# Optimization experiments

Measured on AMD Instinct MI355X. Metric: run time of the kernel, lower is better.

The kernel has to match this reference:

```python
import jax, jax.numpy as jnp
import numpy as np

N_EMB = 1024
HEAD = 64
BLOCK = 2048
BATCH = 8


def setup_inputs() -> dict:
    key = jax.random.key(0)
    k_in, k_q, k_k, k_v = jax.random.split(key, 4)
    inp = jax.random.normal(k_in, (BATCH, BLOCK, N_EMB), dtype=jnp.float32)
    s = 1.0 / np.sqrt(N_EMB)
    Wq = jax.random.uniform(k_q, (N_EMB, HEAD), dtype=jnp.float32, minval=-s, maxval=s)
    Wk = jax.random.uniform(k_k, (N_EMB, HEAD), dtype=jnp.float32, minval=-s, maxval=s)
    Wv = jax.random.uniform(k_v, (N_EMB, HEAD), dtype=jnp.float32, minval=-s, maxval=s)
    return {"input": inp, "Wq": Wq, "Wk": Wk, "Wv": Wv}


def reference(input, Wq, Wk, Wv):
    # input: [B, T, E]; projections to head_size H
    q = jnp.einsum('bte,eh->bth', input, Wq)
    k = jnp.einsum('bte,eh->bth', input, Wk)
    v = jnp.einsum('bte,eh->bth', input, Wv)
    scale = 1.0 / np.sqrt(HEAD).astype(np.float32)
    # [B, T, T] causal scores
    scores = jnp.einsum('bqh,bkh->bqk', q, k) * scale
    T = input.shape[1]
    causal = jnp.tril(jnp.ones((T, T), dtype=bool))
    scores = jnp.where(causal, scores, jnp.float32(-jnp.inf))
    wei = jax.nn.softmax(scores, axis=-1)
    # dropout is identity in eval mode (p=0.1 omitted for deterministic reference)
    return jnp.einsum('bqk,bkh->bqh', wei, v)
```

## Files before the change

### kernel.cpp

```cpp
#include <hip/hip_runtime.h>
#include <hip/hip_bf16.h>
#include <math.h>

#define BATCH 8
#define SEQ   2048
#define EMB   1024
#define HEAD  64
#define BT    (BATCH * SEQ)

typedef __attribute__((ext_vector_type(8))) short  short8;
typedef __attribute__((ext_vector_type(4))) float  floatx4;

__device__ __forceinline__ unsigned short f2bf(float x) {
    union { __hip_bfloat16 h; unsigned short u; } cv;
    cv.h = __float2bfloat16(x);
    return cv.u;
}

__global__ __launch_bounds__(256) void wt_prep(
    const float* __restrict__ Wq, const float* __restrict__ Wk,
    const float* __restrict__ Wv, unsigned short* __restrict__ WT)
{
    __shared__ float tile[64][65];
    const int w  = blockIdx.x >> 4;
    const int k0 = (blockIdx.x & 15) * 64;
    const float* W = (w == 0) ? Wq : (w == 1) ? Wk : Wv;
    const int tid = threadIdx.x;

    for (int idx = tid; idx < 4096; idx += 256) {
        const int kr = idx >> 6, n = idx & 63;
        tile[kr][n] = W[(size_t)(k0 + kr) * HEAD + n];
    }
    __syncthreads();
    const int n  = tid >> 2;
    const int k8 = (tid & 3) * 16;
    unsigned short* dst = WT + (size_t)(w * 64 + n) * EMB + k0 + k8;
    short8 v0, v1;
#pragma unroll
    for (int j = 0; j < 8; ++j) v0[j] = (short)f2bf(tile[k8 + j][n]);
#pragma unroll
    for (int j = 0; j < 8; ++j) v1[j] = (short)f2bf(tile[k8 + 8 + j][n]);
    *(short8*)(dst)     = v0;
    *(short8*)(dst + 8) = v1;
}

__global__ __launch_bounds__(256) void qkv_mfma(
    const float* __restrict__ X, const unsigned short* __restrict__ WT,
    unsigned short* __restrict__ Q, unsigned short* __restrict__ K,
    unsigned short* __restrict__ VT)
{
    const int tid = threadIdx.x;
    const int l   = tid & 63;
    const int wv  = tid >> 6;
    const int wm  = wv >> 1, wn = wv & 1;
    const int g   = l >> 4,  q  = l & 15;
    const int arow = blockIdx.x * 32 + wm * 16 + q;

    floatx4 acc[6];
#pragma unroll
    for (int nt = 0; nt < 6; ++nt) acc[nt] = (floatx4){0.f, 0.f, 0.f, 0.f};

    const float*          xp = X  + (size_t)arow * EMB + g * 8;
    const unsigned short* wp = WT + (size_t)(wn * 96 + q) * EMB + g * 8;

    float4 xa = *(const float4*)(xp);
    float4 xb = *(const float4*)(xp + 4);
    short8 w[6];
#pragma unroll
    for (int nt = 0; nt < 6; ++nt) w[nt] = *(const short8*)(wp + (size_t)nt * 16 * EMB);

    for (int k0 = 0; k0 < EMB - 32; k0 += 32) {
        float4 xa2 = *(const float4*)(xp + 32);
        float4 xb2 = *(const float4*)(xp + 36);
        short8 w2[6];
#pragma unroll
        for (int nt = 0; nt < 6; ++nt) w2[nt] = *(const short8*)(wp + 32 + (size_t)nt * 16 * EMB);
        xp += 32; wp += 32;

        short8 a;
        a[0] = (short)f2bf(xa.x); a[1] = (short)f2bf(xa.y);
        a[2] = (short)f2bf(xa.z); a[3] = (short)f2bf(xa.w);
        a[4] = (short)f2bf(xb.x); a[5] = (short)f2bf(xb.y);
        a[6] = (short)f2bf(xb.z); a[7] = (short)f2bf(xb.w);
#pragma unroll
        for (int nt = 0; nt < 6; ++nt)
            acc[nt] = __builtin_amdgcn_mfma_f32_16x16x32_bf16(a, w[nt], acc[nt], 0, 0, 0);

        xa = xa2; xb = xb2;
#pragma unroll
        for (int nt = 0; nt < 6; ++nt) w[nt] = w2[nt];
    }
    {
        short8 a;
        a[0] = (short)f2bf(xa.x); a[1] = (short)f2bf(xa.y);
        a[2] = (short)f2bf(xa.z); a[3] = (short)f2bf(xa.w);
        a[4] = (short)f2bf(xb.x); a[5] = (short)f2bf(xb.y);
        a[6] = (short)f2bf(xb.z); a[7] = (short)f2bf(xb.w);
#pragma unroll
        for (int nt = 0; nt < 6; ++nt)
            acc[nt] = __builtin_amdgcn_mfma_f32_16x16x32_bf16(a, w[nt], acc[nt], 0, 0, 0);
    }

    const int trow0 = blockIdx.x * 32 + wm * 16 + g * 4;
#pragma unroll
    for (int nt = 0; nt < 6; ++nt) {
        const int c = wn * 96 + nt * 16 + q;
#pragma unroll
        for (int r = 0; r < 4; ++r) {
            const unsigned short v = f2bf(acc[nt][r]);
            const int t = trow0 + r;
            if (c < 64) {
                Q[(size_t)t * HEAD + c] = v;
            } else if (c < 128) {
                K[(size_t)t * HEAD + (c - 64)] = v;
            } else {
                const int bb = t >> 11, tl = t & (SEQ - 1);
                VT[((size_t)bb * HEAD + (c - 128)) * SEQ + tl] = v;
            }
        }
    }
}

__global__ __launch_bounds__(128) void attn_mfma(
    const unsigned short* __restrict__ Q, const unsigned short* __restrict__ K,
    const unsigned short* __restrict__ VT, float* __restrict__ O)
{
    __shared__ unsigned short Ks[2][64][72];
    __shared__ unsigned short Vs[2][64][72];
    __shared__ unsigned short Ps[32][72];

    const int tid = threadIdx.x;
    const int l   = tid & 63;
    const int wv  = tid >> 6;
    const int g   = l >> 4, q = l & 15;
    const int qt  = 63 - (blockIdx.x >> 3);
    const int b   = blockIdx.x & 7;
    const int qrow0 = qt * 32 + wv * 16;
    const size_t kbase = (size_t)b * SEQ * HEAD;
    const size_t vbase = (size_t)b * HEAD * SEQ;

    short8 bq[2];
#pragma unroll
    for (int dc = 0; dc < 2; ++dc)
        bq[dc] = *(const short8*)&Q[kbase + (size_t)(qrow0 + q) * HEAD + dc * 32 + g * 8];

    floatx4 o[4];
#pragma unroll
    for (int dt = 0; dt < 4; ++dt) o[dt] = (floatx4){0.f, 0.f, 0.f, 0.f};
    float m_run = -INFINITY, l_run = 0.f;

    const int nkt = (qt >> 1) + 1;

    short8 kreg[4], vreg[4];
#pragma unroll
    for (int i = 0; i < 4; ++i) {
        const int c = tid + i * 128, r = c >> 3, k8 = (c & 7) * 8;
        kreg[i] = *(const short8*)&K [kbase + (size_t)r * HEAD + k8];
        vreg[i] = *(const short8*)&VT[vbase + (size_t)r * SEQ  + k8];
    }

    for (int kt = 0; kt < nkt; ++kt) {
        const int bs = kt & 1;
#pragma unroll
        for (int i = 0; i < 4; ++i) {
            const int c = tid + i * 128, r = c >> 3, k8 = (c & 7) * 8;
            *(short8*)&Ks[bs][r][k8] = kreg[i];
            *(short8*)&Vs[bs][r][k8] = vreg[i];
        }
        __syncthreads();

        if (kt + 1 < nkt) {
#pragma unroll
            for (int i = 0; i < 4; ++i) {
                const int c = tid + i * 128, r = c >> 3, k8 = (c & 7) * 8;
                kreg[i] = *(const short8*)&K [kbase + (size_t)((kt + 1) * 64 + r) * HEAD + k8];
                vreg[i] = *(const short8*)&VT[vbase + (size_t)r * SEQ + (kt + 1) * 64 + k8];
            }
        }

        floatx4 s[4];
#pragma unroll
        for (int t = 0; t < 4; ++t) {
            s[t] = (floatx4){0.f, 0.f, 0.f, 0.f};
#pragma unroll
            for (int dc = 0; dc < 2; ++dc) {
                const short8 ak = *(const short8*)&Ks[bs][t * 16 + q][dc * 32 + g * 8];
                s[t] = __builtin_amdgcn_mfma_f32_16x16x32_bf16(ak, bq[dc], s[t], 0, 0, 0);
            }
        }

        float sv[4][4];
        if (kt == nkt - 1) {
#pragma unroll
            for (int t = 0; t < 4; ++t)
#pragma unroll
                for (int r = 0; r < 4; ++r) {
                    const int kg = kt * 64 + t * 16 + g * 4 + r;
                    sv[t][r] = (kg > qrow0 + q) ? -INFINITY : s[t][r] * 0.125f;
                }
        } else {
#pragma unroll
            for (int t = 0; t < 4; ++t)
#pragma unroll
                for (int r = 0; r < 4; ++r) sv[t][r] = s[t][r] * 0.125f;
        }

        float pm = -INFINITY;
#pragma unroll
        for (int t = 0; t < 4; ++t)
#pragma unroll
            for (int r = 0; r < 4; ++r) pm = fmaxf(pm, sv[t][r]);
        pm = fmaxf(pm, __shfl_xor(pm, 16));
        pm = fmaxf(pm, __shfl_xor(pm, 32));
        const float mnew = fmaxf(m_run, pm);
        const float crow = __expf(m_run - mnew);
        float p[4][4];
        float psum = 0.f;
#pragma unroll
        for (int t = 0; t < 4; ++t)
#pragma unroll
            for (int r = 0; r < 4; ++r) {
                p[t][r] = __expf(sv[t][r] - mnew);
                psum += p[t][r];
            }
        psum += __shfl_xor(psum, 16);
        psum += __shfl_xor(psum, 32);
        l_run = l_run * crow + psum;
        m_run = mnew;

#pragma unroll
        for (int r = 0; r < 4; ++r) {
            const float cr = __shfl(crow, g * 4 + r);
#pragma unroll
            for (int dt = 0; dt < 4; ++dt) o[dt][r] *= cr;
        }

#pragma unroll
        for (int t = 0; t < 4; ++t) {
            const unsigned int lo = (unsigned)f2bf(p[t][0]) | ((unsigned)f2bf(p[t][1]) << 16);
            const unsigned int hi = (unsigned)f2bf(p[t][2]) | ((unsigned)f2bf(p[t][3]) << 16);
            *(unsigned int*)&Ps[wv * 16 + q][t * 16 + g * 4]     = lo;
            *(unsigned int*)&Ps[wv * 16 + q][t * 16 + g * 4 + 2] = hi;
        }
        asm volatile("s_waitcnt lgkmcnt(0)" ::: "memory");
        __builtin_amdgcn_sched_barrier(0);

#pragma unroll
        for (int kc = 0; kc < 2; ++kc) {
            const short8 pa = *(const short8*)&Ps[wv * 16 + q][kc * 32 + g * 8];
#pragma unroll
            for (int dt = 0; dt < 4; ++dt) {
                const short8 vb = *(const short8*)&Vs[bs][dt * 16 + q][kc * 32 + g * 8];
                o[dt] = __builtin_amdgcn_mfma_f32_16x16x32_bf16(pa, vb, o[dt], 0, 0, 0);
            }
        }
    }

    float lr[4];
#pragma unroll
    for (int r = 0; r < 4; ++r) lr[r] = __shfl(l_run, g * 4 + r);
    const size_t obase = (size_t)b * SEQ * HEAD;
#pragma unroll
    for (int dt = 0; dt < 4; ++dt)
#pragma unroll
        for (int r = 0; r < 4; ++r)
            O[obase + (size_t)(qrow0 + g * 4 + r) * HEAD + dt * 16 + q] = o[dt][r] / lr[r];
}

extern "C" void kernel_launch(void* const* d_in, const int* in_sizes, int n_in,
                              void* d_out, int out_size, void* d_ws, size_t ws_size,
                              hipStream_t stream)
{
    const float* X  = (const float*)d_in[0];
    const float* Wq = (const float*)d_in[1];
    const float* Wk = (const float*)d_in[2];
    const float* Wv = (const float*)d_in[3];
    float* O = (float*)d_out;

    unsigned short* Qb = (unsigned short*)d_ws;
    unsigned short* Kb = Qb + (size_t)BT * HEAD;
    unsigned short* Vt = Kb + (size_t)BT * HEAD;
    unsigned short* WT = Vt + (size_t)BT * HEAD;

    wt_prep <<<dim3(48),  dim3(256), 0, stream>>>(Wq, Wk, Wv, WT);
    qkv_mfma<<<dim3(512), dim3(256), 0, stream>>>(X, WT, Qb, Kb, Vt);
    attn_mfma<<<dim3(512), dim3(128), 0, stream>>>(Qb, Kb, Vt, O);
}
```

Measured before the change: 188.2 us.

## Split attention KV tiles across two wave pairs and halve QKV row tile

The attention kernel now runs four waves per block. Two wave pairs each take alternate KV tiles, and their online-softmax partial results are merged through shared memory at the end, which is a split-K style flash-attention. The QKV projection kernel now gives each block 16 rows, with each wave covering 48 output columns, so twice as many blocks launch. Both changes aim to raise parallelism and occupancy on a 512-block grid, at the cost of extra shared memory, a final merge step, and idle pairs on alternating tiles.

```diff
diff --git a/kernel.cpp b/kernel.cpp
--- a/kernel.cpp
+++ b/kernel.cpp
@@ -52,29 +52,28 @@
     const int tid = threadIdx.x;
     const int l   = tid & 63;
     const int wv  = tid >> 6;
-    const int wm  = wv >> 1, wn = wv & 1;
     const int g   = l >> 4,  q  = l & 15;
-    const int arow = blockIdx.x * 32 + wm * 16 + q;
-
-    floatx4 acc[6];
-#pragma unroll
-    for (int nt = 0; nt < 6; ++nt) acc[nt] = (floatx4){0.f, 0.f, 0.f, 0.f};
+    const int arow = blockIdx.x * 16 + q;
+
+    floatx4 acc[3];
+#pragma unroll
+    for (int nt = 0; nt < 3; ++nt) acc[nt] = (floatx4){0.f, 0.f, 0.f, 0.f};
 
     const float*          xp = X  + (size_t)arow * EMB + g * 8;
-    const unsigned short* wp = WT + (size_t)(wn * 96 + q) * EMB + g * 8;
+    const unsigned short* wp = WT + (size_t)(wv * 48 + q) * EMB + g * 8;
 
     float4 xa = *(const float4*)(xp);
     float4 xb = *(const float4*)(xp + 4);
-    short8 w[6];
-#pragma unroll
-    for (int nt = 0; nt < 6; ++nt) w[nt] = *(const short8*)(wp + (size_t)nt * 16 * EMB);
+    short8 w[3];
+#pragma unroll
+    for (int nt = 0; nt < 3; ++nt) w[nt] = *(const short8*)(wp + (size_t)nt * 16 * EMB);
 
     for (int k0 = 0; k0 < EMB - 32; k0 += 32) {
         float4 xa2 = *(const float4*)(xp + 32);
         float4 xb2 = *(const float4*)(xp + 36);
-        short8 w2[6];
-#pragma unroll
-        for (int nt = 0; nt < 6; ++nt) w2[nt] = *(const short8*)(wp + 32 + (size_t)nt * 16 * EMB);
+        short8 w2[3];
+#pragma unroll
+        for (int nt = 0; nt < 3; ++nt) w2[nt] = *(const short8*)(wp + 32 + (size_t)nt * 16 * EMB);
         xp += 32; wp += 32;
 
         short8 a;
@@ -83,12 +82,12 @@
         a[4] = (short)f2bf(xb.x); a[5] = (short)f2bf(xb.y);
         a[6] = (short)f2bf(xb.z); a[7] = (short)f2bf(xb.w);
 #pragma unroll
-        for (int nt = 0; nt < 6; ++nt)
+        for (int nt = 0; nt < 3; ++nt)
             acc[nt] = __builtin_amdgcn_mfma_f32_16x16x32_bf16(a, w[nt], acc[nt], 0, 0, 0);
 
         xa = xa2; xb = xb2;
 #pragma unroll
-        for (int nt = 0; nt < 6; ++nt) w[nt] = w2[nt];
+        for (int nt = 0; nt < 3; ++nt) w[nt] = w2[nt];
     }
     {
         short8 a;
@@ -97,14 +96,14 @@
         a[4] = (short)f2bf(xb.x); a[5] = (short)f2bf(xb.y);
         a[6] = (short)f2bf(xb.z); a[7] = (short)f2bf(xb.w);
 #pragma unroll
-        for (int nt = 0; nt < 6; ++nt)
+        for (int nt = 0; nt < 3; ++nt)
             acc[nt] = __builtin_amdgcn_mfma_f32_16x16x32_bf16(a, w[nt], acc[nt], 0, 0, 0);
     }
 
-    const int trow0 = blockIdx.x * 32 + wm * 16 + g * 4;
-#pragma unroll
-    for (int nt = 0; nt < 6; ++nt) {
-        const int c = wn * 96 + nt * 16 + q;
+    const int trow0 = blockIdx.x * 16 + g * 4;
+#pragma unroll
+    for (int nt = 0; nt < 3; ++nt) {
+        const int c = wv * 48 + nt * 16 + q;
 #pragma unroll
         for (int r = 0; r < 4; ++r) {
             const unsigned short v = f2bf(acc[nt][r]);
@@ -121,21 +120,24 @@
     }
 }
 
-__global__ __launch_bounds__(128) void attn_mfma(
+__global__ __launch_bounds__(256) void attn_mfma(
     const unsigned short* __restrict__ Q, const unsigned short* __restrict__ K,
     const unsigned short* __restrict__ VT, float* __restrict__ O)
 {
     __shared__ unsigned short Ks[2][64][72];
     __shared__ unsigned short Vs[2][64][72];
-    __shared__ unsigned short Ps[32][72];
-
-    const int tid = threadIdx.x;
-    const int l   = tid & 63;
-    const int wv  = tid >> 6;
-    const int g   = l >> 4, q = l & 15;
-    const int qt  = 63 - (blockIdx.x >> 3);
-    const int b   = blockIdx.x & 7;
-    const int qrow0 = qt * 32 + wv * 16;
+    __shared__ unsigned short Ps[64][72];
+    __shared__ float Mo[2][16][68];
+    __shared__ float Mm[2][16], Ml[2][16];
+
+    const int tid  = threadIdx.x;
+    const int l    = tid & 63;
+    const int wv   = tid >> 6;
+    const int pair = wv >> 1, sub = wv & 1;
+    const int g    = l >> 4, q = l & 15;
+    const int qt   = 63 - (blockIdx.x >> 3);
+    const int b    = blockIdx.x & 7;
+    const int qrow0 = qt * 32 + sub * 16;
     const size_t kbase = (size_t)b * SEQ * HEAD;
     const size_t vbase = (size_t)b * HEAD * SEQ;
 
@@ -151,10 +153,10 @@
 
     const int nkt = (qt >> 1) + 1;
 
-    short8 kreg[4], vreg[4];
-#pragma unroll
-    for (int i = 0; i < 4; ++i) {
-        const int c = tid + i * 128, r = c >> 3, k8 = (c & 7) * 8;
+    short8 kreg[2], vreg[2];
+#pragma unroll
+    for (int i = 0; i < 2; ++i) {
+        const int c = tid + i * 256, r = c >> 3, k8 = (c & 7) * 8;
         kreg[i] = *(const short8*)&K [kbase + (size_t)r * HEAD + k8];
         vreg[i] = *(const short8*)&VT[vbase + (size_t)r * SEQ  + k8];
     }
@@ -162,8 +164,8 @@
     for (int kt = 0; kt < nkt; ++kt) {
         const int bs = kt & 1;
 #pragma unroll
-        for (int i = 0; i < 4; ++i) {
-            const int c = tid + i * 128, r = c >> 3, k8 = (c & 7) * 8;
+        for (int i = 0; i < 2; ++i) {
+            const int c = tid + i * 256, r = c >> 3, k8 = (c & 7) * 8;
             *(short8*)&Ks[bs][r][k8] = kreg[i];
             *(short8*)&Vs[bs][r][k8] = vreg[i];
         }
@@ -171,100 +173,124 @@
 
         if (kt + 1 < nkt) {
 #pragma unroll
-            for (int i = 0; i < 4; ++i) {
-                const int c = tid + i * 128, r = c >> 3, k8 = (c & 7) * 8;
+            for (int i = 0; i < 2; ++i) {
+                const int c = tid + i * 256, r = c >> 3, k8 = (c & 7) * 8;
                 kreg[i] = *(const short8*)&K [kbase + (size_t)((kt + 1) * 64 + r) * HEAD + k8];
                 vreg[i] = *(const short8*)&VT[vbase + (size_t)r * SEQ + (kt + 1) * 64 + k8];
             }
         }
 
-        floatx4 s[4];
-#pragma unroll
-        for (int t = 0; t < 4; ++t) {
-            s[t] = (floatx4){0.f, 0.f, 0.f, 0.f};
-#pragma unroll
-            for (int dc = 0; dc < 2; ++dc) {
-                const short8 ak = *(const short8*)&Ks[bs][t * 16 + q][dc * 32 + g * 8];
-                s[t] = __builtin_amdgcn_mfma_f32_16x16x32_bf16(ak, bq[dc], s[t], 0, 0, 0);
-            }
-        }
-
-        float sv[4][4];
-        if (kt == nkt - 1) {
+        if ((kt & 1) == pair) {
+            floatx4 s[4];
+#pragma unroll
+            for (int t = 0; t < 4; ++t) {
+                s[t] = (floatx4){0.f, 0.f, 0.f, 0.f};
+#pragma unroll
+                for (int dc = 0; dc < 2; ++dc) {
+                    const short8 ak = *(const short8*)&Ks[bs][t * 16 + q][dc * 32 + g * 8];
+                    s[t] = __builtin_amdgcn_mfma_f32_16x16x32_bf16(ak, bq[dc], s[t], 0, 0, 0);
+                }
+            }
+
+            float sv[4][4];
+            if (kt == nkt - 1) {
+#pragma unroll
+                for (int t = 0; t < 4; ++t)
+#pragma unroll
+                    for (int r = 0; r < 4; ++r) {
+                        const int kg = kt * 64 + t * 16 + g * 4 + r;
+                        sv[t][r] = (kg > qrow0 + q) ? -INFINITY : s[t][r] * 0.125f;
+                    }
+            } else {
+#pragma unroll
+                for (int t = 0; t < 4; ++t)
+#pragma unroll
+                    for (int r = 0; r < 4; ++r) sv[t][r] = s[t][r] * 0.125f;
+            }
+
+            float pm = -INFINITY;
 #pragma unroll
             for (int t = 0; t < 4; ++t)
 #pragma unroll
+                for (int r = 0; r < 4; ++r) pm = fmaxf(pm, sv[t][r]);
+            pm = fmaxf(pm, __shfl_xor(pm, 16));
+            pm = fmaxf(pm, __shfl_xor(pm, 32));
+            const float mnew = fmaxf(m_run, pm);
+            const float crow = __expf(m_run - mnew);
+            float p[4][4];
+            float psum = 0.f;
+#pragma unroll
+            for (int t = 0; t < 4; ++t)
+#pragma unroll
                 for (int r = 0; r < 4; ++r) {
-                    const int kg = kt * 64 + t * 16 + g * 4 + r;
-                    sv[t][r] = (kg > qrow0 + q) ? -INFINITY : s[t][r] * 0.125f;
+                    p[t][r] = __expf(sv[t][r] - mnew);
+                    psum += p[t][r];
                 }
-        } else {
-#pragma unroll
-            for (int t = 0; t < 4; ++t)
-#pragma unroll
-                for (int r = 0; r < 4; ++r) sv[t][r] = s[t][r] * 0.125f;
-        }
-
-        float pm = -INFINITY;
-#pragma unroll
-        for (int t = 0; t < 4; ++t)
-#pragma unroll
-            for (int r = 0; r < 4; ++r) pm = fmaxf(pm, sv[t][r]);
-        pm = fmaxf(pm, __shfl_xor(pm, 16));
-        pm = fmaxf(pm, __shfl_xor(pm, 32));
-        const float mnew = fmaxf(m_run, pm);
-        const float crow = __expf(m_run - mnew);
-        float p[4][4];
-        float psum = 0.f;
-#pragma unroll
-        for (int t = 0; t < 4; ++t)
+            psum += __shfl_xor(psum, 16);
+            psum += __shfl_xor(psum, 32);
+            l_run = l_run * crow + psum;
+            m_run = mnew;
+
 #pragma unroll
             for (int r = 0; r < 4; ++r) {
-                p[t][r] = __expf(sv[t][r] - mnew);
-                psum += p[t][r];
-            }
-        psum += __shfl_xor(psum, 16);
-        psum += __shfl_xor(psum, 32);
-        l_run = l_run * crow + psum;
-        m_run = mnew;
-
+                const float cr = __shfl(crow, g * 4 + r);
+#pragma unroll
+                for (int dt = 0; dt < 4; ++dt) o[dt][r] *= cr;
+            }
+
+#pragma unroll
+            for (int t = 0; t < 4; ++t) {
+                const unsigned int lo = (unsigned)f2bf(p[t][0]) | ((unsigned)f2bf(p[t][1]) << 16);
+                const unsigned int hi = (unsigned)f2bf(p[t][2]) | ((unsigned)f2bf(p[t][3]) << 16);
+                *(unsigned int*)&Ps[wv * 16 + q][t * 16 + g * 4]     = lo;
+                *(unsigned int*)&Ps[wv * 16 + q][t * 16 + g * 4 + 2] = hi;
+            }
+            asm volatile("s_waitcnt lgkmcnt(0)" ::: "memory");
+            __builtin_amdgcn_sched_barrier(0);
+
+#pragma unroll
+            for (int kc = 0; kc < 2; ++kc) {
+                const short8 pa = *(const short8*)&Ps[wv * 16 + q][kc * 32 + g * 8];
+#pragma unroll
+                for (int dt = 0; dt < 4; ++dt) {
+                    const short8 vb = *(const short8*)&Vs[bs][dt * 16 + q][kc * 32 + g * 8];
+                    o[dt] = __builtin_amdgcn_mfma_f32_16x16x32_bf16(pa, vb, o[dt], 0, 0, 0);
+                }
+            }
+        }
+    }
+
+    __syncthreads();
+    if (pair == 1) {
+#pragma unroll
+        for (int dt = 0; dt < 4; ++dt)
+#pragma unroll
+            for (int r = 0; r < 4; ++r)
+                Mo[sub][g * 4 + r][dt * 16 + q] = o[dt][r];
+        if (g == 0) { Mm[sub][q] = m_run; Ml[sub][q] = l_run; }
+    }
+    __syncthreads();
+    if (pair == 0) {
+        const float m1  = Mm[sub][q];
+        const float l1v = Ml[sub][q];
+        const float mx  = fmaxf(m_run, m1);
+        const float c0  = __expf(m_run - mx);
+        const float c1  = __expf(m1 - mx);
+        const float lm  = l_run * c0 + l1v * c1;
+        const size_t obase = (size_t)b * SEQ * HEAD;
 #pragma unroll
         for (int r = 0; r < 4; ++r) {
-            const float cr = __shfl(crow, g * 4 + r);
-#pragma unroll
-            for (int dt = 0; dt < 4; ++dt) o[dt][r] *= cr;
-        }
-
-#pragma unroll
-        for (int t = 0; t < 4; ++t) {
-            const unsigned int lo = (unsigned)f2bf(p[t][0]) | ((unsigned)f2bf(p[t][1]) << 16);
-            const unsigned int hi = (unsigned)f2bf(p[t][2]) | ((unsigned)f2bf(p[t][3]) << 16);
-            *(unsigned int*)&Ps[wv * 16 + q][t * 16 + g * 4]     = lo;
-            *(unsigned int*)&Ps[wv * 16 + q][t * 16 + g * 4 + 2] = hi;
-        }
-        asm volatile("s_waitcnt lgkmcnt(0)" ::: "memory");
-        __builtin_amdgcn_sched_barrier(0);
-
-#pragma unroll
-        for (int kc = 0; kc < 2; ++kc) {
-            const short8 pa = *(const short8*)&Ps[wv * 16 + q][kc * 32 + g * 8];
+            const float c0r = __shfl(c0, g * 4 + r);
+            const float c1r = __shfl(c1, g * 4 + r);
+            const float lr  = __shfl(lm, g * 4 + r);
+            const float inv = 1.0f / lr;
 #pragma unroll
             for (int dt = 0; dt < 4; ++dt) {
-                const short8 vb = *(const short8*)&Vs[bs][dt * 16 + q][kc * 32 + g * 8];
-                o[dt] = __builtin_amdgcn_mfma_f32_16x16x32_bf16(pa, vb, o[dt], 0, 0, 0);
-            }
-        }
-    }
-
-    float lr[4];
-#pragma unroll
-    for (int r = 0; r < 4; ++r) lr[r] = __shfl(l_run, g * 4 + r);
-    const size_t obase = (size_t)b * SEQ * HEAD;
-#pragma unroll
-    for (int dt = 0; dt < 4; ++dt)
-#pragma unroll
-        for (int r = 0; r < 4; ++r)
-            O[obase + (size_t)(qrow0 + g * 4 + r) * HEAD + dt * 16 + q] = o[dt][r] / lr[r];
+                const float val = o[dt][r] * c0r + Mo[sub][g * 4 + r][dt * 16 + q] * c1r;
+                O[obase + (size_t)(qrow0 + g * 4 + r) * HEAD + dt * 16 + q] = val * inv;
+            }
+        }
+    }
 }
 
 extern "C" void kernel_launch(void* const* d_in, const int* in_sizes, int n_in,
@@ -282,7 +308,7 @@
     unsigned short* Vt = Kb + (size_t)BT * HEAD;
     unsigned short* WT = Vt + (size_t)BT * HEAD;
 
-    wt_prep <<<dim3(48),  dim3(256), 0, stream>>>(Wq, Wk, Wv, WT);
-    qkv_mfma<<<dim3(512), dim3(256), 0, stream>>>(X, WT, Qb, Kb, Vt);
-    attn_mfma<<<dim3(512), dim3(128), 0, stream>>>(Qb, Kb, Vt, O);
-}
+    wt_prep  <<<dim3(48),   dim3(256), 0, stream>>>(Wq, Wk, Wv, WT);
+    qkv_mfma <<<dim3(1024), dim3(256), 0, stream>>>(X, WT, Qb, Kb, Vt);
+    attn_mfma<<<dim3(512),  dim3(256), 0, stream>>>(Qb, Kb, Vt, O);
+}
```

Result: slower. 198.3 us (+5.4%).
